# Kernel optimization log

Measured on AMD Instinct MI355X. Metric: run time of the kernel, lower is better.

The kernel has to match this reference:

```python
import jax, jax.numpy as jnp
import numpy as np

B, T, D = 4, 2048, 1024
H = 16
HD = D // H  # 64

def setup_inputs() -> dict:
    key = jax.random.key(0)
    ks = jax.random.split(key, 5)
    x = jax.random.normal(ks[0], (B, T, D), dtype=jnp.float32)
    # Linear params, torch default init scale ~ U(-1/sqrt(fan_in), 1/sqrt(fan_in))
    s = 1.0 / np.sqrt(D)
    W_qkv = jax.random.uniform(ks[1], (D, 3 * D), jnp.float32, -s, s)
    b_qkv = jax.random.uniform(ks[2], (3 * D,), jnp.float32, -s, s)
    W_proj = jax.random.uniform(ks[3], (D, D), jnp.float32, -s, s)
    b_proj = jax.random.uniform(ks[4], (D,), jnp.float32, -s, s)
    return {"x": x, "W_qkv": W_qkv, "b_qkv": b_qkv, "W_proj": W_proj, "b_proj": b_proj}

def reference(x, W_qkv, b_qkv, W_proj, b_proj):
    b, t, c = x.shape
    qkv = x @ W_qkv + b_qkv                       # [B,T,3D]
    q, k, v = jnp.split(qkv, 3, axis=-1)
    # [B,T,D] -> [B,H,T,HD]
    def heads(a):
        return a.reshape(b, t, H, HD).transpose(0, 2, 1, 3)
    q, k, v = heads(q), heads(k), heads(v)
    scale = 1.0 / jnp.sqrt(jnp.float32(HD))
    att = jnp.einsum('bhqd,bhkd->bhqk', q, k) * scale   # [B,H,T,T]
    causal = jnp.tril(jnp.ones((t, t), dtype=bool))
    att = jnp.where(causal, att, -jnp.inf)
    att = jax.nn.softmax(att, axis=-1)
    out = jnp.einsum('bhqk,bhkd->bhqd', att, v)          # [B,H,T,HD]
    out = out.transpose(0, 2, 1, 3).reshape(b, t, c)
    return out @ W_proj + b_proj
```

## Files before the change

### kernel.cpp

```cpp
#include <hip/hip_runtime.h>
#include <hip/hip_bf16.h>
#include <stdint.h>

using u16 = unsigned short;
using u32t = unsigned int;
typedef __bf16 bf16x8 __attribute__((ext_vector_type(8)));
typedef float f32x4 __attribute__((ext_vector_type(4)));
typedef float f32x16 __attribute__((ext_vector_type(16)));

#define SEQ_T 2048
#define DM 1024
#define NH 16
#define HD 64
#define NB 4

__device__ inline u16 f2bfu(float f) {
    __hip_bfloat16 h = __float2bfloat16(f);
    return __builtin_bit_cast(u16, h);
}

__device__ inline bf16x8 ld_frag(const u16* p) {
    return __builtin_bit_cast(bf16x8, *reinterpret_cast<const uint4*>(p));
}

__device__ inline void gload_lds16(const u16* g, u16* l) {
    __builtin_amdgcn_global_load_lds(
        (const __attribute__((address_space(1))) void*)g,
        (__attribute__((address_space(3))) void*)l, 16, 0, 0);
}

__device__ inline float fexp2(float x) { return __builtin_amdgcn_exp2f(x); }

__global__ __launch_bounds__(256) void cvt_x_kernel(const float* __restrict__ x,
                                                    u16* __restrict__ o) {
    size_t i = (size_t)blockIdx.x * 256 + threadIdx.x;
    const float4* xv = reinterpret_cast<const float4*>(x);
    float4 a = xv[2 * i];
    float4 b = xv[2 * i + 1];
    u16 r[8] = {f2bfu(a.x), f2bfu(a.y), f2bfu(a.z), f2bfu(a.w),
                f2bfu(b.x), f2bfu(b.y), f2bfu(b.z), f2bfu(b.w)};
    *reinterpret_cast<uint4*>(o + i * 8) = *reinterpret_cast<const uint4*>(r);
}

__global__ __launch_bounds__(256) void trans_w(const float* __restrict__ W,
                                               u16* __restrict__ Wt,
                                               int K, int N) {
    __shared__ __align__(16) float tile[64][72];
    int k0 = blockIdx.y * 64, n0 = blockIdx.x * 64;
    int tid = threadIdx.x;
#pragma unroll
    for (int p = 0; p < 4; ++p) {
        int idx = p * 256 + tid;
        int r = idx >> 4, c = (idx & 15) * 4;
        float4 v = *reinterpret_cast<const float4*>(&W[(size_t)(k0 + r) * N + n0 + c]);
        *reinterpret_cast<float4*>(&tile[r][c]) = v;
    }
    __syncthreads();
#pragma unroll
    for (int p = 0; p < 4; ++p) {
        int idx = p * 256 + tid;
        int nr = idx >> 4, kg = (idx & 15) * 4;
        u16 u[4];
#pragma unroll
        for (int j = 0; j < 4; ++j) u[j] = f2bfu(tile[kg + j][nr]);
        *reinterpret_cast<uint2*>(&Wt[(size_t)(n0 + nr) * K + k0 + kg]) =
            *reinterpret_cast<const uint2*>(u);
    }
}

template <int F32OUT, int SCALEQ>
__global__ __launch_bounds__(256, 3) void gemm_r4(const u16* __restrict__ A,
                                                  const u16* __restrict__ Bt,
                                                  const float* __restrict__ bias,
                                                  float* __restrict__ Cf,
                                                  u16* __restrict__ Cb,
                                                  int M, int N, int K) {
    __shared__ __align__(16) u16 smem[24576];
    const int tid = threadIdx.x;
    const int wid = tid >> 6, lane = tid & 63;
    const int llo = lane & 15, lhi = lane >> 4;
    const int wm = wid >> 1, wn = wid & 1;
    const int cpx = gridDim.x >> 3;
    const int swz = (blockIdx.x & 7) * cpx + (blockIdx.x >> 3);
    const int nb = N >> 7;
    const int m0 = (swz / nb) << 7, n0 = (swz % nb) << 7;
    const int T = K >> 5;

    f32x4 acc[4][4];
#pragma unroll
    for (int i = 0; i < 4; ++i)
#pragma unroll
        for (int j = 0; j < 4; ++j) acc[i][j] = (f32x4){0.f, 0.f, 0.f, 0.f};

    auto stage = [&](int t, int sb) {
        const int kb = t << 5;
#pragma unroll
        for (int j = 0; j < 2; ++j) {
            int c = j * 256 + tid;
            int row = c >> 2, kc = (c & 3) * 8;
            gload_lds16(A + (size_t)(m0 + row) * K + kb + kc, smem + sb + c * 8);
        }
#pragma unroll
        for (int j = 0; j < 2; ++j) {
            int c = j * 256 + tid;
            int row = c >> 2, kc = (c & 3) * 8;
            gload_lds16(Bt + (size_t)(n0 + row) * K + kb + kc,
                        smem + sb + 4096 + c * 8);
        }
    };

    stage(0, 0);
    stage(1, 8192);

    for (int t = 0; t < T; ++t) {
        if (t == T - 1)
            asm volatile("s_waitcnt vmcnt(0)" ::: "memory");
        else
            asm volatile("s_waitcnt vmcnt(4)" ::: "memory");
        __builtin_amdgcn_sched_barrier(0);
        __builtin_amdgcn_s_barrier();
        __builtin_amdgcn_sched_barrier(0);
        const u16* Ab = smem + (t % 3) * 8192;
        const u16* Bb = Ab + 4096;
        bf16x8 af[4], bfr[4];
#pragma unroll
        for (int mf = 0; mf < 4; ++mf)
            af[mf] = ld_frag(Ab + (wm * 64 + mf * 16 + llo) * 32 + lhi * 8);
#pragma unroll
        for (int nf = 0; nf < 4; ++nf)
            bfr[nf] = ld_frag(Bb + (wn * 64 + nf * 16 + llo) * 32 + lhi * 8);
        if (t + 2 < T) stage(t + 2, ((t + 2) % 3) * 8192);
        __builtin_amdgcn_s_setprio(1);
#pragma unroll
        for (int mf = 0; mf < 4; ++mf)
#pragma unroll
            for (int nf = 0; nf < 4; ++nf)
                acc[mf][nf] = __builtin_amdgcn_mfma_f32_16x16x32_bf16(
                    af[mf], bfr[nf], acc[mf][nf], 0, 0, 0);
        __builtin_amdgcn_s_setprio(0);
    }

    const float SC2 = 0.18033688f;
    const int row_base = m0 + wm * 64;
    const int col_base = n0 + wn * 64;
#pragma unroll
    for (int nf = 0; nf < 4; ++nf) {
        int col = col_base + nf * 16 + llo;
        float bv = bias[col];
        const bool doScale = SCALEQ && (col < 1024);
#pragma unroll
        for (int mf = 0; mf < 4; ++mf) {
#pragma unroll
            for (int r = 0; r < 4; ++r) {
                int row = row_base + mf * 16 + lhi * 4 + r;
                float v = acc[mf][nf][r] + bv;
                if (doScale) v *= SC2;
                if (F32OUT)
                    Cf[(size_t)row * N + col] = v;
                else
                    Cb[(size_t)row * N + col] = f2bfu(v);
            }
        }
    }
}

__global__ __launch_bounds__(512, 2) void attn_kernel(const u16* __restrict__ qkv,
                                                      u16* __restrict__ o) {
    __shared__ __align__(16) u16 smem[34048];
    const int bid = blockIdx.x;
    const int amap[8] = {7, 5, 3, 1, 6, 4, 2, 0};
    const int bh = bid & 63;
    const int qc = amap[bid >> 6];
    const int b = bh >> 4, h = bh & 15;
    const int tid = threadIdx.x;
    const int wid = tid >> 6, lane = tid & 63;
    const int l31 = lane & 31, lh = lane >> 5;
    const u16* base = qkv + (size_t)b * SEQ_T * (3 * DM);
    const int qrow0 = qc * 256 + wid * 32;
    const int q_abs = qrow0 + l31;
    const int nkv2 = 2 * qc + 2;

    bf16x8 qf[4];
    {
        const u16* qp = base + (size_t)q_abs * (3 * DM) + h * HD + lh * 8;
#pragma unroll
        for (int km = 0; km < 4; ++km) qf[km] = ld_frag(qp + km * 16);
    }

    f32x16 oac0, oac1;
#pragma unroll
    for (int r = 0; r < 16; ++r) { oac0[r] = 0.f; oac1[r] = 0.f; }
    float m_run = -1e30f, l_run = 0.f;

    uint4 va, vb;
    const int vpr = tid >> 3, vm = tid & 7;

    auto stageK = [&](int kb2, int bi2) {
#pragma unroll
        for (int p = 0; p < 2; ++p) {
            int kv = p * 64 + wid * 8 + (lane >> 3);
            int cl = lane & 7;
            const u16* src = base + (size_t)(kb2 * 128 + kv) * (3 * DM) + DM + h * HD +
                             ((cl ^ (kv & 7)) * 8);
            gload_lds16(src, smem + bi2 * 8320 + (p * 8 + wid) * 520);
        }
    };
    auto loadV = [&](int kb2) {
        const u16* vp =
            base + (size_t)(kb2 * 128 + 2 * vpr) * (3 * DM) + 2 * DM + h * HD + vm * 8;
        va = *reinterpret_cast<const uint4*>(vp);
        vb = *reinterpret_cast<const uint4*>(vp + 3 * DM);
    };
    auto writeV = [&](int bi2) {
        u16 ua[8], ub[8];
        *reinterpret_cast<uint4*>(ua) = va;
        *reinterpret_cast<uint4*>(ub) = vb;
        const int cbk = vpr >> 2, off = 2 * (vpr & 3);
        const int sw = (2 * vm) & 7;
        u16* vt = smem + 16640 + bi2 * 8704;
#pragma unroll
        for (int j = 0; j < 8; ++j) {
            int d = vm * 8 + j;
            u32t val = (u32t)ua[j] | ((u32t)ub[j] << 16);
            *reinterpret_cast<u32t*>(vt + d * 136 + ((cbk ^ sw) * 8) + off) = val;
        }
    };

    loadV(0);
    stageK(0, 0);
    writeV(0);
    asm volatile("s_waitcnt lgkmcnt(0)" ::: "memory");
    asm volatile("s_waitcnt vmcnt(1)" ::: "memory");
    __builtin_amdgcn_sched_barrier(0);
    __builtin_amdgcn_s_barrier();
    __builtin_amdgcn_sched_barrier(0);

    const int vsw = (2 * (l31 >> 3)) & 7;
    const int qmax = qrow0 + 31;
    const int krow0 = (l31 >> 3) * 520 + (l31 & 7) * 64;
    const int krow1 = (4 + (l31 >> 3)) * 520 + (l31 & 7) * 64;

    for (int kb2 = 0; kb2 < nkv2; ++kb2) {
        const int cur = kb2 & 1;
        const bool pre = (kb2 + 1 < nkv2);
        if (pre) { loadV(kb2 + 1); stageK(kb2 + 1, cur ^ 1); }

#pragma unroll
        for (int s = 0; s < 2; ++s) {
            if (s == 1) {
                if (pre) asm volatile("s_waitcnt vmcnt(4)" ::: "memory");
                else     asm volatile("s_waitcnt vmcnt(0)" ::: "memory");
                __builtin_amdgcn_sched_barrier(0);
            }
            const int kv0 = kb2 * 128 + s * 64;
            if (kv0 > qmax) continue;
            f32x16 s0, s1;
#pragma unroll
            for (int r = 0; r < 16; ++r) { s0[r] = 0.f; s1[r] = 0.f; }
            const u16* kbase = smem + cur * 8320 + s * 4160;
#pragma unroll
            for (int km = 0; km < 4; ++km) {
                bf16x8 kf = ld_frag(kbase + krow0 + (((km * 2 + lh) ^ (l31 & 7)) * 8));
                s0 = __builtin_amdgcn_mfma_f32_32x32x16_bf16(kf, qf[km], s0, 0, 0, 0);
            }
#pragma unroll
            for (int km = 0; km < 4; ++km) {
                bf16x8 kf = ld_frag(kbase + krow1 + (((km * 2 + lh) ^ (l31 & 7)) * 8));
                s1 = __builtin_amdgcn_mfma_f32_32x32x16_bf16(kf, qf[km], s1, 0, 0, 0);
            }

            if (kv0 + 63 > qrow0) {
#pragma unroll
                for (int r = 0; r < 16; ++r) {
                    int ka = kv0 + (r & 3) + 8 * (r >> 2) + 4 * lh;
                    if (ka > q_abs) s0[r] = -1e30f;
                    if (ka + 32 > q_abs) s1[r] = -1e30f;
                }
            }

            float t16[16];
#pragma unroll
            for (int r = 0; r < 16; ++r) t16[r] = fmaxf(s0[r], s1[r]);
#pragma unroll
            for (int r = 0; r < 8; ++r) t16[r] = fmaxf(t16[r], t16[r + 8]);
#pragma unroll
            for (int r = 0; r < 4; ++r) t16[r] = fmaxf(t16[r], t16[r + 4]);
            float pm = fmaxf(fmaxf(t16[0], t16[1]), fmaxf(t16[2], t16[3]));
            pm = fmaxf(pm, __shfl_xor(pm, 32));
            if (!__all(pm - m_run <= 8.f)) {
                const float mnew = fmaxf(m_run, pm);
                const float sc = fexp2(m_run - mnew);
                m_run = mnew;
                l_run *= sc;
#pragma unroll
                for (int r = 0; r < 16; ++r) { oac0[r] *= sc; oac1[r] *= sc; }
            }
            float a16[16];
#pragma unroll
            for (int r = 0; r < 16; ++r) { s0[r] = fexp2(s0[r] - m_run); }
#pragma unroll
            for (int r = 0; r < 16; ++r) { s1[r] = fexp2(s1[r] - m_run); }
#pragma unroll
            for (int r = 0; r < 16; ++r) a16[r] = s0[r] + s1[r];
#pragma unroll
            for (int r = 0; r < 8; ++r) a16[r] += a16[r + 8];
#pragma unroll
            for (int r = 0; r < 4; ++r) a16[r] += a16[r + 4];
            float sum = (a16[0] + a16[1]) + (a16[2] + a16[3]);
            sum += __shfl_xor(sum, 32);
            l_run += sum;

            u32t pk0[8], pk1[8];
#pragma unroll
            for (int w = 0; w < 8; ++w) {
                float a0 = s0[2 * w], b0 = s0[2 * w + 1];
                float a1 = s1[2 * w], b1 = s1[2 * w + 1];
                asm("v_cvt_pk_bf16_f32 %0, %1, %2" : "=v"(pk0[w]) : "v"(a0), "v"(b0));
                asm("v_cvt_pk_bf16_f32 %0, %1, %2" : "=v"(pk1[w]) : "v"(a1), "v"(b1));
            }
            asm("v_permlane32_swap_b32 %0, %1" : "+v"(pk0[0]), "+v"(pk0[2]));
            asm("v_permlane32_swap_b32 %0, %1" : "+v"(pk0[1]), "+v"(pk0[3]));
            asm("v_permlane32_swap_b32 %0, %1" : "+v"(pk0[4]), "+v"(pk0[6]));
            asm("v_permlane32_swap_b32 %0, %1" : "+v"(pk0[5]), "+v"(pk0[7]));
            asm("v_permlane32_swap_b32 %0, %1" : "+v"(pk1[0]), "+v"(pk1[2]));
            asm("v_permlane32_swap_b32 %0, %1" : "+v"(pk1[1]), "+v"(pk1[3]));
            asm("v_permlane32_swap_b32 %0, %1" : "+v"(pk1[4]), "+v"(pk1[6]));
            asm("v_permlane32_swap_b32 %0, %1" : "+v"(pk1[5]), "+v"(pk1[7]));
            bf16x8 pf[4];
            {
                uint4 t0 = {pk0[0], pk0[1], pk0[2], pk0[3]};
                uint4 t1 = {pk0[4], pk0[5], pk0[6], pk0[7]};
                uint4 t2 = {pk1[0], pk1[1], pk1[2], pk1[3]};
                uint4 t3 = {pk1[4], pk1[5], pk1[6], pk1[7]};
                pf[0] = __builtin_bit_cast(bf16x8, t0);
                pf[1] = __builtin_bit_cast(bf16x8, t1);
                pf[2] = __builtin_bit_cast(bf16x8, t2);
                pf[3] = __builtin_bit_cast(bf16x8, t3);
            }

            const u16* vbase = smem + 16640 + cur * 8704;
#pragma unroll
            for (int km = 0; km < 4; ++km) {
                bf16x8 vf = ld_frag(vbase + l31 * 136 +
                                    ((s * 8 + ((km * 2 + lh) ^ vsw)) * 8));
                oac0 = __builtin_amdgcn_mfma_f32_32x32x16_bf16(vf, pf[km], oac0, 0, 0, 0);
            }
#pragma unroll
            for (int km = 0; km < 4; ++km) {
                bf16x8 vf = ld_frag(vbase + (32 + l31) * 136 +
                                    ((s * 8 + ((km * 2 + lh) ^ vsw)) * 8));
                oac1 = __builtin_amdgcn_mfma_f32_32x32x16_bf16(vf, pf[km], oac1, 0, 0, 0);
            }
        }

        if (pre) {
            writeV(cur ^ 1);
            asm volatile("s_waitcnt lgkmcnt(0)" ::: "memory");
            asm volatile("s_waitcnt vmcnt(1)" ::: "memory");
        } else {
            asm volatile("s_waitcnt lgkmcnt(0)" ::: "memory");
        }
        __builtin_amdgcn_sched_barrier(0);
        __builtin_amdgcn_s_barrier();
        __builtin_amdgcn_sched_barrier(0);
    }

    const float inv = 1.f / l_run;
    u16* osh = smem + wid * 2240;
#pragma unroll
    for (int r = 0; r < 16; ++r) {
        int dl = (r & 3) + 8 * (r >> 2) + 4 * lh;
        osh[l31 * 70 + dl] = f2bfu(oac0[r] * inv);
        osh[l31 * 70 + 32 + dl] = f2bfu(oac1[r] * inv);
    }
    __syncthreads();
    {
        const u16* rs = osh + l31 * 70 + lh * 32;
        u16* op = o + (size_t)(b * SEQ_T + qrow0 + l31) * DM + h * HD + lh * 32;
        u32t w[16];
#pragma unroll
        for (int i = 0; i < 16; ++i) w[i] = *reinterpret_cast<const u32t*>(rs + i * 2);
#pragma unroll
        for (int i = 0; i < 4; ++i) {
            uint4 t = {w[4 * i], w[4 * i + 1], w[4 * i + 2], w[4 * i + 3]};
            *reinterpret_cast<uint4*>(op + 8 * i) = t;
        }
    }
}

extern "C" void kernel_launch(void* const* d_in, const int* in_sizes, int n_in,
                              void* d_out, int out_size, void* d_ws, size_t ws_size,
                              hipStream_t stream) {
    const float* x = (const float*)d_in[0];
    const float* Wqkv = (const float*)d_in[1];
    const float* bqkv = (const float*)d_in[2];
    const float* Wproj = (const float*)d_in[3];
    const float* bproj = (const float*)d_in[4];
    float* out = (float*)d_out;
    char* ws = (char*)d_ws;

    u16* xb   = (u16*)(ws);
    u16* wtq  = (u16*)(ws + 16777216);
    u16* wtp  = (u16*)(ws + 23068672);
    u16* qkvb = (u16*)(ws + 25165824);
    u16* ob   = (u16*)(ws + 75497472);

    cvt_x_kernel<<<4096, 256, 0, stream>>>(x, xb);
    trans_w<<<dim3(3072 / 64, 1024 / 64), 256, 0, stream>>>(Wqkv, wtq, 1024, 3072);
    trans_w<<<dim3(1024 / 64, 1024 / 64), 256, 0, stream>>>(Wproj, wtp, 1024, 1024);

    gemm_r4<0, 1><<<1536, 256, 0, stream>>>(
        xb, wtq, bqkv, nullptr, qkvb, 8192, 3072, 1024);

    attn_kernel<<<512, 512, 0, stream>>>(qkvb, ob);

    gemm_r4<1, 0><<<512, 256, 0, stream>>>(
        ob, wtp, bproj, out, nullptr, 8192, 1024, 1024);
}
```

Baseline: 172.1 us.

## Use 256x128-tile triple-buffered GEMM with 512 threads for QKV projection

```diff
diff --git a/kernel.cpp b/kernel.cpp
--- a/kernel.cpp
+++ b/kernel.cpp
@@ -65,6 +65,101 @@
         for (int j = 0; j < 4; ++j) u[j] = f2bfu(tile[kg + j][nr]);
         *reinterpret_cast<uint2*>(&Wt[(size_t)(n0 + nr) * K + k0 + kg]) =
             *reinterpret_cast<const uint2*>(u);
+    }
+}
+
+template <int F32OUT, int SCALEQ>
+__global__ __launch_bounds__(512, 2) void gemm_r3(const u16* __restrict__ A,
+                                                  const u16* __restrict__ Bt,
+                                                  const float* __restrict__ bias,
+                                                  float* __restrict__ Cf,
+                                                  u16* __restrict__ Cb,
+                                                  int M, int N, int K) {
+    __shared__ __align__(16) u16 smem[36864];
+    const int tid = threadIdx.x;
+    const int wid = tid >> 6, lane = tid & 63;
+    const int llo = lane & 15, lhi = lane >> 4;
+    const int wm = wid >> 1, wn = wid & 1;
+    const int cpx = gridDim.x >> 3;
+    const int swz = (blockIdx.x & 7) * cpx + (blockIdx.x >> 3);
+    const int nb = N >> 7;
+    const int m0 = (swz / nb) << 8, n0 = (swz % nb) << 7;
+    const int T = K >> 5;
+
+    f32x4 acc[4][4];
+#pragma unroll
+    for (int i = 0; i < 4; ++i)
+#pragma unroll
+        for (int j = 0; j < 4; ++j) acc[i][j] = (f32x4){0.f, 0.f, 0.f, 0.f};
+
+    auto stage = [&](int t, int sb) {
+        const int kb = t << 5;
+#pragma unroll
+        for (int j = 0; j < 2; ++j) {
+            int c = j * 512 + tid;
+            int row = c >> 2, kc = (c & 3) * 8;
+            gload_lds16(A + (size_t)(m0 + row) * K + kb + kc, smem + sb + c * 8);
+        }
+        {
+            int c = tid;
+            int row = c >> 2, kc = (c & 3) * 8;
+            gload_lds16(Bt + (size_t)(n0 + row) * K + kb + kc,
+                        smem + sb + 8192 + c * 8);
+        }
+    };
+
+    stage(0, 0);
+    stage(1, 12288);
+
+    for (int t = 0; t < T; ++t) {
+        if (t == T - 1)
+            asm volatile("s_waitcnt vmcnt(0)" ::: "memory");
+        else
+            asm volatile("s_waitcnt vmcnt(3)" ::: "memory");
+        __builtin_amdgcn_sched_barrier(0);
+        __builtin_amdgcn_s_barrier();
+        __builtin_amdgcn_sched_barrier(0);
+        const u16* Ab = smem + (t % 3) * 12288;
+        const u16* Bb = Ab + 8192;
+        bf16x8 af[4], bfr[4];
+#pragma unroll
+        for (int mf = 0; mf < 4; ++mf)
+            af[mf] = ld_frag(Ab + (wm * 64 + mf * 16 + llo) * 32 + lhi * 8);
+#pragma unroll
+        for (int nf = 0; nf < 4; ++nf)
+            bfr[nf] = ld_frag(Bb + (wn * 64 + nf * 16 + llo) * 32 + lhi * 8);
+        if (t + 2 < T) stage(t + 2, ((t + 2) % 3) * 12288);
+        __builtin_amdgcn_s_setprio(1);
+#pragma unroll
+        for (int mf = 0; mf < 4; ++mf)
+#pragma unroll
+            for (int nf = 0; nf < 4; ++nf)
+                acc[mf][nf] = __builtin_amdgcn_mfma_f32_16x16x32_bf16(
+                    af[mf], bfr[nf], acc[mf][nf], 0, 0, 0);
+        __builtin_amdgcn_s_setprio(0);
+    }
+
+    const float SC2 = 0.18033688f;
+    const int row_base = m0 + wm * 64;
+    const int col_base = n0 + wn * 64;
+#pragma unroll
+    for (int nf = 0; nf < 4; ++nf) {
+        int col = col_base + nf * 16 + llo;
+        float bv = bias[col];
+        const bool doScale = SCALEQ && (col < 1024);
+#pragma unroll
+        for (int mf = 0; mf < 4; ++mf) {
+#pragma unroll
+            for (int r = 0; r < 4; ++r) {
+                int row = row_base + mf * 16 + lhi * 4 + r;
+                float v = acc[mf][nf][r] + bv;
+                if (doScale) v *= SC2;
+                if (F32OUT)
+                    Cf[(size_t)row * N + col] = v;
+                else
+                    Cb[(size_t)row * N + col] = f2bfu(v);
+            }
+        }
     }
 }
 
@@ -409,7 +504,7 @@
     trans_w<<<dim3(3072 / 64, 1024 / 64), 256, 0, stream>>>(Wqkv, wtq, 1024, 3072);
     trans_w<<<dim3(1024 / 64, 1024 / 64), 256, 0, stream>>>(Wproj, wtp, 1024, 1024);
 
-    gemm_r4<0, 1><<<1536, 256, 0, stream>>>(
+    gemm_r3<0, 1><<<768, 512, 0, stream>>>(
         xb, wtq, bqkv, nullptr, qkvb, 8192, 3072, 1024);
 
     attn_kernel<<<512, 512, 0, stream>>>(qkvb, ob);
```

Result: faster. 162.5 us (-5.6%).
